# Optimization experiments

Hardware: AMD Instinct MI355X
Metric: run time of the kernel (lower is better)

Reference implementation:

```python
import jax, jax.numpy as jnp
import numpy as np

NUM_CLASSES = 2
THRESHOLD = 0.35
NEGPOS_RATIO = 7
VARIANCES = (0.1, 0.2)
B, P, O = 64, 16800, 64  # batch, num_priors, num_objs per image


def point_form(pr):
    # cxcywh -> xyxy
    return jnp.concatenate([pr[:, :2] - pr[:, 2:] / 2, pr[:, :2] + pr[:, 2:] / 2], axis=1)


def jaccard(a, b):
    # a: [A,4] xyxy, b: [Bx,4] xyxy -> IoU [A,Bx]
    lt = jnp.maximum(a[:, None, :2], b[None, :, :2])
    rb = jnp.minimum(a[:, None, 2:], b[None, :, 2:])
    wh = jnp.clip(rb - lt, 0.0)
    inter = wh[..., 0] * wh[..., 1]
    area_a = ((a[:, 2] - a[:, 0]) * (a[:, 3] - a[:, 1]))[:, None]
    area_b = ((b[:, 2] - b[:, 0]) * (b[:, 3] - b[:, 1]))[None, :]
    return inter / (area_a + area_b - inter)


def encode(matched, priors):
    # matched xyxy [P,4], priors cxcywh [P,4]
    g_cxcy = (matched[:, :2] + matched[:, 2:]) / 2 - priors[:, :2]
    g_cxcy = g_cxcy / (VARIANCES[0] * priors[:, 2:])
    g_wh = (matched[:, 2:] - matched[:, :2]) / priors[:, 2:]
    g_wh = jnp.log(g_wh) / VARIANCES[1]
    return jnp.concatenate([g_cxcy, g_wh], axis=1)


def encode_landm(matched, priors):
    # matched [P,10] -> [P,5,2]
    m = matched.reshape(-1, 5, 2)
    g = (m - priors[:, None, :2]) / (VARIANCES[0] * priors[:, None, 2:])
    return g.reshape(-1, 10)


def match_one(truths, labels, landms, priors):
    # truths [O,4], labels [O], landms [O,10]
    overlaps = jaccard(truths, point_form(priors))  # [O,P]
    best_prior_overlap = overlaps.max(axis=1)       # per-gt best IoU
    best_prior_idx = overlaps.argmax(axis=1)
    valid_gt = best_prior_overlap >= 0.2
    best_truth_overlap = overlaps.max(axis=0)       # per-prior best IoU
    best_truth_idx = overlaps.argmax(axis=0)
    # index_fill(2) only for valid gts (best_prior_idx_filter)
    bto = best_truth_overlap.at[best_prior_idx].set(
        jnp.where(valid_gt, 2.0, best_truth_overlap[best_prior_idx]))
    # ensure every gt keeps its best prior
    bti = best_truth_idx.at[best_prior_idx].set(jnp.arange(truths.shape[0]))
    matches = truths[bti]                  # [P,4]
    conf = labels[bti]                     # [P]
    conf = jnp.where(bto < THRESHOLD, 0.0, conf)
    loc = encode(matches, priors)
    landm = encode_landm(landms[bti], priors)
    return loc, conf, landm


def smooth_l1_sum(x, mask):
    ax = jnp.abs(x)
    v = jnp.where(ax < 1.0, 0.5 * ax * ax, ax - 0.5)
    return (v * mask).sum()


def setup_inputs() -> dict:
    key = jax.random.key(0)
    k1, k2, k3, k4, k5, k6, k7, k8 = jax.random.split(key, 8)
    loc_data = jax.random.normal(k1, (B, P, 4), jnp.float32)
    conf_data = jax.random.normal(k2, (B, P, NUM_CLASSES), jnp.float32)
    landm_data = jax.random.normal(k3, (B, P, 10), jnp.float32)
    # priors: cx,cy in (0,1), w,h in (0.02,0.22)
    cxy = jax.random.uniform(k4, (P, 2), jnp.float32)
    wh = jax.random.uniform(k5, (P, 2), jnp.float32) * 0.2 + 0.02
    priors = jnp.concatenate([cxy, wh], axis=1)
    # targets: valid corner boxes + landmarks + label in {1,-1}
    xy1 = jax.random.uniform(k6, (B, O, 2), jnp.float32) * 0.6
    bwh = jax.random.uniform(k7, (B, O, 2), jnp.float32) * 0.3 + 0.05
    boxes = jnp.concatenate([xy1, xy1 + bwh], axis=-1)
    lms = jax.random.uniform(k8, (B, O, 10), jnp.float32)
    lab = jnp.where(jax.random.uniform(jax.random.fold_in(key, 9), (B, O, 1)) < 0.3, -1.0, 1.0)
    targets = jnp.concatenate([boxes, lms, lab], axis=-1)
    return {"loc_data": loc_data, "conf_data": conf_data, "landm_data": landm_data,
            "priors": priors, "targets": targets}


def reference(loc_data, conf_data, landm_data, priors, targets):
    num = loc_data.shape[0]
    num_priors = priors.shape[0]
    truths = targets[:, :, :4]
    landms = targets[:, :, 4:14]
    labels = targets[:, :, -1]
    loc_t, conf_t, landm_t = jax.vmap(match_one, in_axes=(0, 0, 0, None))(
        truths, labels, landms, priors)  # [B,P,4], [B,P], [B,P,10]

    # landmark loss over conf_t > 0
    pos1 = conf_t > 0
    num_pos_landm = pos1.astype(jnp.int32).sum(axis=1, keepdims=True)
    N1 = jnp.maximum(num_pos_landm.sum().astype(jnp.float32), 1.0)
    loss_landm = smooth_l1_sum(landm_data - landm_t, pos1[..., None].astype(landm_data.dtype))

    # localization loss over conf_t != 0 ; conf_t[pos] = 1
    pos = conf_t != 0
    conf_t01 = jnp.where(pos, 1, 0)  # int {0,1}
    loss_l = smooth_l1_sum(loc_data - loc_t, pos[..., None].astype(loc_data.dtype))

    # hard negative mining on per-prior CE loss (global-max log_sum_exp, as in source)
    batch_conf = conf_data.reshape(-1, NUM_CLASSES)
    x_max = batch_conf.max()
    lse = jnp.log(jnp.exp(batch_conf - x_max).sum(axis=1, keepdims=True)) + x_max
    gathered = jnp.take_along_axis(batch_conf, conf_t01.reshape(-1, 1), axis=1)
    loss_c = (lse - gathered).reshape(num, -1)  # [B,P]; positives NOT zeroed (as in source)
    loss_idx = jnp.argsort(-loss_c, axis=1)
    idx_rank = jnp.argsort(loss_idx, axis=1)
    num_pos = pos.astype(jnp.int32).sum(axis=1, keepdims=True)  # [B,1]
    num_neg = jnp.minimum(NEGPOS_RATIO * num_pos, num_priors - 1)
    neg = idx_rank < num_neg  # [B,P]
    neg_pos = pos | neg

    # cross-entropy (sum) over selected pos+neg priors
    logp = jax.nn.log_softmax(conf_data, axis=-1)  # [B,P,C]
    ce = -jnp.take_along_axis(logp, conf_t01[..., None], axis=-1)[..., 0]
    loss_c_final = (ce * neg_pos.astype(ce.dtype)).sum()

    N = jnp.maximum(num_pos.sum().astype(jnp.float32), 1.0)
    return (loss_l / N, loss_c_final / N, loss_landm / N1)
```

## Files before the change

kernel.cpp:

```cpp
#include <hip/hip_runtime.h>
#include <math.h>

#define BN 64
#define PN 16800
#define ON 64
#define THRESH 0.35f
#define NEGPOS 7
#define GX 66
#define NBLK (BN * GX)
#define GXB 17
#define NBT (BN * GXB)
#define PT 4
#define TG 4
#define PSPLIT 2
#define PHALF 8400
#define NBP2 (BN * 16 * PSPLIT)
#define KREG 17
#define TAILV (PN - 16 * 1024)
#define NBINS 4096
#define MAXM 4096

struct GAcc {
  unsigned ticket;
  float sl, slm, sc;
  int np, np1;
  unsigned pad0, pad1;
};

__device__ __forceinline__ unsigned f2key(float f) {
  unsigned u = __float_as_uint(f);
  return (u & 0x80000000u) ? ~u : (u | 0x80000000u);
}
__device__ __forceinline__ float key2f(unsigned k) {
  unsigned u = (k & 0x80000000u) ? (k & 0x7FFFFFFFu) : ~k;
  return __uint_as_float(u);
}
__device__ __forceinline__ float sl1(float d) {
  float a = fabsf(d);
  return (a < 1.f) ? 0.5f * a * a : a - 0.5f;
}

__global__ void k_match2(const float* __restrict__ priors,
                         const float* __restrict__ targets,
                         float* __restrict__ bto, int* __restrict__ bti,
                         unsigned long long* __restrict__ bpp,
                         GAcc* __restrict__ gacc) {
  int bid = blockIdx.x;
  int tid = threadIdx.x;

  if (bid < NBT) {
    int b = bid / GXB;
    int slab = bid - b * GXB;
    int base = slab * 1024 + tid;
    if (bid == 0 && tid < 8)
      ((unsigned*)gacc)[tid] = 0;

    __shared__ float4 tbox[ON];
    __shared__ float tarea[ON];
    if (tid < ON) {
      const float* tg = &targets[((long)b * ON + tid) * 15];
      float4 bx = make_float4(tg[0], tg[1], tg[2], tg[3]);
      tbox[tid] = bx;
      tarea[tid] = (bx.z - bx.x) * (bx.w - bx.y);
    }
    __syncthreads();

    float px1[PT], py1[PT], px2[PT], py2[PT], ab[PT];
    bool val[PT];
#pragma unroll
    for (int i = 0; i < PT; i++) {
      int p = base + 256 * i;
      val[i] = p < PN;
      float4 pr = reinterpret_cast<const float4*>(priors)[val[i] ? p : base];
      px1[i] = pr.x - pr.z * 0.5f; py1[i] = pr.y - pr.w * 0.5f;
      px2[i] = pr.x + pr.z * 0.5f; py2[i] = pr.y + pr.w * 0.5f;
      ab[i] = (px2[i] - px1[i]) * (py2[i] - py1[i]);
    }
    float bi[PT], bu[PT]; int id[PT];
#pragma unroll
    for (int i = 0; i < PT; i++) { bi[i] = -1.f; bu[i] = 1.f; id[i] = 0; }

#pragma unroll 4
    for (int t = 0; t < ON; t++) {
      float4 a = tbox[t];
      float aa = tarea[t];
#pragma unroll
      for (int i = 0; i < PT; i++) {
        float lx = fmaxf(a.x, px1[i]), ly = fmaxf(a.y, py1[i]);
        float rx = fminf(a.z, px2[i]), ry = fminf(a.w, py2[i]);
        float w = fmaxf(rx - lx, 0.f), h = fmaxf(ry - ly, 0.f);
        float inter = w * h;
        float uni = aa + ab[i] - inter;
        if (inter * bu[i] > bi[i] * uni) { bi[i] = inter; bu[i] = uni; id[i] = t; }
      }
    }
#pragma unroll
    for (int i = 0; i < PT; i++) {
      if (val[i]) {
        int p = base + 256 * i;
        bto[(long)b * PN + p] = bi[i] / bu[i];
        bti[(long)b * PN + p] = id[i];
      }
    }
  } else {
    int id2 = bid - NBT;
    int b = id2 >> 5;
    int rest = id2 & 31;
    int g = rest >> 1;
    int h = rest & 1;
    int t0 = g * TG;
    float ax1[TG], ay1[TG], ax2[TG], ay2[TG], area_a[TG];
#pragma unroll
    for (int i = 0; i < TG; i++) {
      const float* tg = &targets[((long)b * ON + t0 + i) * 15];
      ax1[i] = tg[0]; ay1[i] = tg[1]; ax2[i] = tg[2]; ay2[i] = tg[3];
      area_a[i] = (ax2[i] - ax1[i]) * (ay2[i] - ay1[i]);
    }
    float bi[TG], bu[TG]; int bp[TG];
#pragma unroll
    for (int i = 0; i < TG; i++) { bi[i] = -1.f; bu[i] = 1.f; bp[i] = 0x7FFFFFFF; }
    int pend = (h + 1) * PHALF;
    for (int p = h * PHALF + tid; p < pend; p += 256) {
      float4 pr = reinterpret_cast<const float4*>(priors)[p];
      float px1 = pr.x - pr.z * 0.5f, py1 = pr.y - pr.w * 0.5f;
      float px2 = pr.x + pr.z * 0.5f, py2 = pr.y + pr.w * 0.5f;
      float area_b = (px2 - px1) * (py2 - py1);
#pragma unroll
      for (int i = 0; i < TG; i++) {
        float lx = fmaxf(ax1[i], px1), ly = fmaxf(ay1[i], py1);
        float rx = fminf(ax2[i], px2), ry = fminf(ay2[i], py2);
        float w = fmaxf(rx - lx, 0.f), h2 = fmaxf(ry - ly, 0.f);
        float inter = w * h2;
        float uni = area_a[i] + area_b - inter;
        if (inter * bu[i] > bi[i] * uni) { bi[i] = inter; bu[i] = uni; bp[i] = p; }
      }
    }
#pragma unroll
    for (int off = 1; off < 64; off <<= 1) {
#pragma unroll
      for (int i = 0; i < TG; i++) {
        float oi = __shfl_xor(bi[i], off), ou = __shfl_xor(bu[i], off);
        int op = __shfl_xor(bp[i], off);
        float a = oi * bu[i], c = bi[i] * ou;
        if (a > c || (a == c && op < bp[i])) { bi[i] = oi; bu[i] = ou; bp[i] = op; }
      }
    }
    __shared__ float si[TG][4], su[TG][4];
    __shared__ int spx[TG][4];
    int w = tid >> 6;
    if ((tid & 63) == 0) {
#pragma unroll
      for (int i = 0; i < TG; i++) { si[i][w] = bi[i]; su[i][w] = bu[i]; spx[i][w] = bp[i]; }
    }
    __syncthreads();
    if (tid < TG) {
      float fi = si[tid][0], fu = su[tid][0]; int fp = spx[tid][0];
      for (int ww = 1; ww < 4; ww++) {
        float a = si[tid][ww] * fu, c = fi * su[tid][ww];
        if (a > c || (a == c && spx[tid][ww] < fp)) { fi = si[tid][ww]; fu = su[tid][ww]; fp = spx[tid][ww]; }
      }
      float q = fi / fu;
      unsigned long long key = ((unsigned long long)f2key(q) << 32) | (unsigned)(~fp);
      bpp[((long)b * ON + t0 + tid) * PSPLIT + h] = key;
    }
  }
}

__global__ void k_encode(const float* __restrict__ loc_data,
                         const float* __restrict__ conf_data,
                         const float* __restrict__ landm_data,
                         const float* __restrict__ priors,
                         const float* __restrict__ targets,
                         const float* __restrict__ bto, const int* __restrict__ bti,
                         const unsigned long long* __restrict__ bpp,
                         float* __restrict__ lossc, unsigned char* __restrict__ posf,
                         float* __restrict__ part_l, float* __restrict__ part_lm,
                         int* __restrict__ np_part, int* __restrict__ np1_part) {
  int b = blockIdx.y;
  int p = blockIdx.x * 256 + threadIdx.x;
  int bid = b * GX + blockIdx.x;
  __shared__ float4 tgs4[ON * 15 / 4];
  __shared__ int ovr[256];
  float* tgs = (float*)tgs4;
  if (threadIdx.x < ON * 15 / 4)
    tgs4[threadIdx.x] = reinterpret_cast<const float4*>(targets + (long)b * ON * 15)[threadIdx.x];
  ovr[threadIdx.x] = -1;
  __syncthreads();
  if (threadIdx.x < ON) {
    int t = threadIdx.x;
    unsigned long long v0 = bpp[((long)b * ON + t) * PSPLIT];
    unsigned long long v1 = bpp[((long)b * ON + t) * PSPLIT + 1];
    unsigned long long best = v0 > v1 ? v0 : v1;
    float q = key2f((unsigned)(best >> 32));
    int qp = (int)(~(unsigned)best);
    int s0 = blockIdx.x * 256;
    if (qp >= s0 && qp < s0 + 256) {
      int valid = (q >= 0.2f) ? 1 : 0;
      atomicMax(&ovr[qp - s0], (t << 1) | valid);
    }
  }
  __syncthreads();

  float sum_l = 0.f, sum_lm = 0.f;
  int cp = 0, cp1 = 0;
  if (p < PN) {
    int t = bti[b * PN + p];
    float ov = bto[b * PN + p];
    int o = ovr[threadIdx.x];
    if (o >= 0) { t = o >> 1; if (o & 1) ov = 2.0f; }
    const float* tg = &tgs[t * 15];
    float label = tg[14];
    bool pos = ov >= THRESH;
    bool pos1 = pos && (label > 0.f);
    float4 pr = reinterpret_cast<const float4*>(priors)[p];
    if (pos) {
      float rz = 1.0f / pr.z, rw = 1.0f / pr.w;
      float m0 = tg[0], m1 = tg[1], m2 = tg[2], m3 = tg[3];
      float g0 = ((m0 + m2) * 0.5f - pr.x) * rz * 10.f;
      float g1 = ((m1 + m3) * 0.5f - pr.y) * rw * 10.f;
      float g2 = __logf((m2 - m0) * rz) * 5.f;
      float g3 = __logf((m3 - m1) * rw) * 5.f;
      const float* ld = &loc_data[((long)b * PN + p) * 4];
      sum_l = sl1(ld[0] - g0) + sl1(ld[1] - g1) + sl1(ld[2] - g2) + sl1(ld[3] - g3);
      cp = 1;
      if (pos1) {
        const float* lm = &landm_data[((long)b * PN + p) * 10];
#pragma unroll
        for (int i = 0; i < 5; i++) {
          float gx = (tg[4 + 2 * i] - pr.x) * rz * 10.f;
          float gy = (tg[5 + 2 * i] - pr.y) * rw * 10.f;
          sum_lm += sl1(lm[2 * i] - gx) + sl1(lm[2 * i + 1] - gy);
        }
        cp1 = 1;
      }
    }
    float2 c2 = reinterpret_cast<const float2*>(conf_data)[(long)b * PN + p];
    float m = fmaxf(c2.x, c2.y);
    float lse = m + __logf(__expf(c2.x - m) + __expf(c2.y - m));
    lossc[b * PN + p] = lse - (pos ? c2.y : c2.x);
    posf[b * PN + p] = pos ? 1 : 0;
  }
  for (int off = 32; off; off >>= 1) {
    sum_l += __shfl_down(sum_l, off);
    sum_lm += __shfl_down(sum_lm, off);
    cp += __shfl_down(cp, off);
    cp1 += __shfl_down(cp1, off);
  }
  __shared__ float sl4[4], slm4[4];
  __shared__ int sp4[4], sp14[4];
  int w = threadIdx.x >> 6;
  if ((threadIdx.x & 63) == 0) { sl4[w] = sum_l; slm4[w] = sum_lm; sp4[w] = cp; sp14[w] = cp1; }
  __syncthreads();
  if (threadIdx.x == 0) {
    part_l[bid] = sl4[0] + sl4[1] + sl4[2] + sl4[3];
    part_lm[bid] = slm4[0] + slm4[1] + slm4[2] + slm4[3];
    np_part[bid] = sp4[0] + sp4[1] + sp4[2] + sp4[3];
    np1_part[bid] = sp14[0] + sp14[1] + sp14[2] + sp14[3];
  }
}

__global__ void __launch_bounds__(1024) k_select(const float* __restrict__ lossc,
                                                 const unsigned char* __restrict__ posf,
                                                 const int* __restrict__ np_part,
                                                 const int* __restrict__ np1_part,
                                                 const float* __restrict__ part_l,
                                                 const float* __restrict__ part_lm,
                                                 GAcc* __restrict__ gacc,
                                                 float* __restrict__ out) {
  int b = blockIdx.x;
  int tid = threadIdx.x;
  int lane = tid & 63;
  int wv = tid >> 6;
  __shared__ unsigned hist[NBINS];
  __shared__ unsigned wtot[16];
  __shared__ float resv[MAXM];
  __shared__ int residx[MAXM];
  __shared__ int s_np, s_B, s_kp;
  __shared__ unsigned s_mc;
  const float* row = &lossc[(long)b * PN];
  const unsigned char* prow = &posf[(long)b * PN];

  if (tid == 0) s_np = 0;
  for (int i = tid; i < NBINS; i += 1024) hist[i] = 0;
  __syncthreads();
  if (tid < GX) atomicAdd(&s_np, np_part[b * GX + tid]);

  bool tailOk = tid < TAILV;
  float vreg[KREG];
  unsigned preg = 0;
#pragma unroll
  for (int r = 0; r < KREG - 1; r++) {
    vreg[r] = row[tid + 1024 * r];
    if (prow[tid + 1024 * r]) preg |= (1u << r);
  }
  vreg[KREG - 1] = tailOk ? row[tid + 1024 * (KREG - 1)] : -1.f;
  if (tailOk && prow[tid + 1024 * (KREG - 1)]) preg |= (1u << (KREG - 1));
  int breg[KREG];
#pragma unroll
  for (int r = 0; r < KREG; r++) {
    int q = (int)(vreg[r] * 256.0f);
    breg[r] = q < 0 ? 0 : (q > NBINS - 1 ? NBINS - 1 : q);
  }
  __syncthreads();
  int np = s_np;
  int k = NEGPOS * np;
  if (k > PN - 1) k = PN - 1;
  bool haveNeg = (k > 0);

  int B = NBINS, kp = 0, m = 0;
  bool allB = false, fallback = false;
  if (haveNeg) {
#pragma unroll
    for (int r = 0; r < KREG; r++)
      if (r < KREG - 1 || tailOk) atomicAdd(&hist[breg[r]], 1u);
    __syncthreads();
    int t4 = tid * 4;
    unsigned h0 = hist[t4], h1 = hist[t4 + 1], h2 = hist[t4 + 2], h3 = hist[t4 + 3];
    unsigned th = h0 + h1 + h2 + h3;
    unsigned v = th;
#pragma unroll
    for (int off = 1; off < 64; off <<= 1) {
      unsigned tv = (unsigned)__shfl_down((int)v, off);
      if (lane + off < 64) v += tv;
    }
    if (lane == 0) wtot[wv] = v;
    __syncthreads();
    unsigned add = 0;
    for (int w2 = wv + 1; w2 < 16; w2++) add += wtot[w2];
    unsigned S_t = v + add;
    unsigned S_next = S_t - th;
    if (S_t >= (unsigned)k && S_next < (unsigned)k) {
      unsigned run = S_next; int Bl; unsigned kpl;
      if (run + h3 >= (unsigned)k) { Bl = t4 + 3; kpl = k - run; }
      else { run += h3;
        if (run + h2 >= (unsigned)k) { Bl = t4 + 2; kpl = k - run; }
        else { run += h2;
          if (run + h1 >= (unsigned)k) { Bl = t4 + 1; kpl = k - run; }
          else { run += h1; Bl = t4; kpl = k - run; } } }
      s_B = Bl; s_kp = (int)kpl;
    }
    __syncthreads();
    B = s_B; kp = s_kp; m = (int)hist[B];
    allB = (kp == m);
    fallback = (!allB && m > MAXM);
  }

  float acc = 0.f;
  if (haveNeg && !allB && !fallback) {
    if (tid == 0) s_mc = 0;
    __syncthreads();
#pragma unroll
    for (int r = 0; r < KREG; r++) {
      if ((r < KREG - 1 || tailOk) && breg[r] == B) {
        unsigned slot = atomicAdd(&s_mc, 1u);
        resv[slot] = vreg[r];
        residx[slot] = (tid + 1024 * r) | (((preg >> r) & 1u) ? 0x40000000 : 0);
      }
    }
    __syncthreads();
    for (int i = tid; i < m; i += 1024) {
      float vi = resv[i];
      int pk = residx[i];
      int ii = pk & 0x3FFFFFFF;
      bool posi = (pk & 0x40000000) != 0;
      int rank = 0;
      for (int j = 0; j < m; j++) {
        float vj = resv[j];
        int ij = residx[j] & 0x3FFFFFFF;
        rank += (vj > vi || (vj == vi && ij < ii)) ? 1 : 0;
      }
      if (rank < kp && !posi) acc += vi;
    }
  }

  unsigned T = 0, R = 0, C = 0;
  if (fallback) {
    __shared__ unsigned s_lo, s_hi, fcnt[16];
    if (tid == 0) { s_lo = 0u; s_hi = 0xFFFFFFFFu; }
    __syncthreads();
    for (int it = 0; it < 32; it++) {
      unsigned lo = s_lo, hi = s_hi;
      unsigned mid = lo + ((hi - lo) >> 1) + ((hi - lo) & 1u);
      unsigned c = 0;
#pragma unroll
      for (int r = 0; r < KREG; r++)
        if (r < KREG - 1 || tailOk) c += (f2key(vreg[r]) >= mid) ? 1u : 0u;
#pragma unroll
      for (int o = 32; o; o >>= 1) c += (unsigned)__shfl_down((int)c, o);
      if (lane == 0) fcnt[wv] = c;
      __syncthreads();
      if (tid == 0) {
        unsigned tot = 0;
        for (int i = 0; i < 16; i++) tot += fcnt[i];
        if (tot >= (unsigned)k) s_lo = mid; else s_hi = mid - 1;
      }
      __syncthreads();
      if (s_lo >= s_hi) break;
    }
    T = s_lo;
    unsigned cg = 0, ce = 0;
#pragma unroll
    for (int r = 0; r < KREG; r++) {
      if (r < KREG - 1 || tailOk) {
        unsigned key = f2key(vreg[r]);
        cg += (key > T) ? 1u : 0u;
        ce += (key == T) ? 1u : 0u;
      }
    }
#pragma unroll
    for (int o = 32; o; o >>= 1) {
      cg += (unsigned)__shfl_down((int)cg, o);
      ce += (unsigned)__shfl_down((int)ce, o);
    }
    if (lane == 0) { fcnt[wv] = cg; wtot[wv] = ce; }
    __syncthreads();
    if (tid == 0) {
      unsigned tg2 = 0, te = 0;
      for (int i = 0; i < 16; i++) { tg2 += fcnt[i]; te += wtot[i]; }
      fcnt[0] = tg2; wtot[0] = te;
    }
    __syncthreads();
    C = wtot[0];
    R = (unsigned)k - fcnt[0];
    if (C != R && tid < 64) {
      unsigned running = 0;
      for (int base2 = 0; base2 < PN; base2 += 64) {
        int p = base2 + tid;
        bool tie = false, pos = false;
        float v2 = 0.f;
        if (p < PN) { v2 = row[p]; tie = (f2key(v2) == T); pos = prow[p] != 0; }
        unsigned long long mm = __ballot(tie);
        if (tie) {
          unsigned rank = running + (unsigned)__popcll(mm & ((1ull << tid) - 1));
          if (rank < R && !pos) acc += v2;
        }
        running += (unsigned)__popcll(mm);
      }
    }
  }

  unsigned ptc = 0;
#pragma unroll
  for (int r = 0; r < KREG; r++) {
    if (r < KREG - 1 || tailOk) {
      float v2 = vreg[r];
      bool pos = (preg >> r) & 1u;
      if (pos) acc += v2;
      else if (haveNeg) {
        if (!fallback) {
          if (breg[r] > B || (breg[r] == B && allB)) acc += v2;
        } else {
          if (f2key(v2) > T) acc += v2;
        }
      }
      if (fallback && pos && f2key(v2) == T) ptc++;
    }
  }
  for (int o = 32; o; o >>= 1) {
    acc += __shfl_down(acc, o);
    ptc += __shfl_down(ptc, o);
  }
  __shared__ float wsum[16];
  __shared__ unsigned wpt[16];
  if (lane == 0) { wsum[wv] = acc; wpt[wv] = ptc; }
  __syncthreads();

  __shared__ float s_rsl, s_rslm;
  __shared__ int s_rnp1;
  if (tid == 0) { s_rsl = 0.f; s_rslm = 0.f; s_rnp1 = 0; }
  __syncthreads();
  if (tid < GX) {
    atomicAdd(&s_rsl, part_l[b * GX + tid]);
    atomicAdd(&s_rslm, part_lm[b * GX + tid]);
    atomicAdd(&s_rnp1, np1_part[b * GX + tid]);
  }
  __syncthreads();

  if (tid == 0) {
    float tot = 0.f; unsigned pt = 0;
    for (int i = 0; i < 16; i++) { tot += wsum[i]; pt += wpt[i]; }
    if (fallback && C == R) tot += (float)(C - pt) * key2f(T);
    atomicAdd(&gacc->sc, tot);
    atomicAdd(&gacc->sl, s_rsl);
    atomicAdd(&gacc->slm, s_rslm);
    atomicAdd(&gacc->np, np);
    atomicAdd(&gacc->np1, s_rnp1);
  }
  __threadfence();
  __shared__ int lastF;
  if (tid == 0) lastF = (atomicAdd(&gacc->ticket, 1u) == (unsigned)(BN - 1)) ? 1 : 0;
  __syncthreads();
  if (lastF && tid == 0) {
    __threadfence();
    float sl = atomicAdd(&gacc->sl, 0.f);
    float slm = atomicAdd(&gacc->slm, 0.f);
    float sc = atomicAdd(&gacc->sc, 0.f);
    int tnp = atomicAdd(&gacc->np, 0);
    int tnp1 = atomicAdd(&gacc->np1, 0);
    float N = fmaxf((float)tnp, 1.f);
    float N1 = fmaxf((float)tnp1, 1.f);
    out[0] = sl / N;
    out[1] = sc / N;
    out[2] = slm / N1;
  }
}

extern "C" void kernel_launch(void* const* d_in, const int* in_sizes, int n_in,
                              void* d_out, int out_size, void* d_ws, size_t ws_size,
                              hipStream_t stream) {
  const float* loc_data = (const float*)d_in[0];
  const float* conf_data = (const float*)d_in[1];
  const float* landm_data = (const float*)d_in[2];
  const float* priors = (const float*)d_in[3];
  const float* targets = (const float*)d_in[4];
  float* out = (float*)d_out;

  char* ws = (char*)d_ws;
  const size_t SZ = (size_t)BN * PN * 4;
  size_t off = 0;
  float* lossc = (float*)(ws + off); off += SZ;
  float* bto = (float*)(ws + off); off += SZ;
  int* bti = (int*)(ws + off); off += SZ;
  unsigned char* posf = (unsigned char*)(ws + off); off += (size_t)BN * PN;
  off = (off + 15) & ~(size_t)15;
  unsigned long long* bpp = (unsigned long long*)(ws + off);
  off += (size_t)BN * ON * PSPLIT * 8;
  float* part_l = (float*)(ws + off); off += NBLK * 4;
  float* part_lm = (float*)(ws + off); off += NBLK * 4;
  int* np_part = (int*)(ws + off); off += NBLK * 4;
  int* np1_part = (int*)(ws + off); off += NBLK * 4;
  GAcc* gacc = (GAcc*)(ws + off); off += sizeof(GAcc);

  dim3 gbp(GX, BN);

  k_match2<<<NBT + NBP2, 256, 0, stream>>>(priors, targets, bto, bti, bpp, gacc);
  k_encode<<<gbp, 256, 0, stream>>>(loc_data, conf_data, landm_data, priors, targets,
                                    bto, bti, bpp, lossc, posf,
                                    part_l, part_lm, np_part, np1_part);
  k_select<<<BN, 1024, 0, stream>>>(lossc, posf, np_part, np1_part, part_l, part_lm,
                                    gacc, out);
}
```

Measured before the change: 209.4 us.

## Fuse encode stage into match kernel and apply best-prior overrides as deltas in select

Removes the separate k_encode kernel. The per-prior match blocks now compute the loc/landmark smooth-L1 partials, the per-prior CE loss and the positive flags directly from their own argmax results. The per-gt best-prior overrides are moved into k_select, which recomputes the changed priors' contributions as deltas and patches the loss and positive values through a shared-memory bitmap and lookup. This saves one launch and one global round trip over bto/bti, but adds serial fix-up work and a per-element bitmap check in the select kernel.

```diff
diff --git a/kernel.cpp b/kernel.cpp
--- a/kernel.cpp
+++ b/kernel.cpp
@@ -6,8 +6,6 @@
 #define ON 64
 #define THRESH 0.35f
 #define NEGPOS 7
-#define GX 66
-#define NBLK (BN * GX)
 #define GXB 17
 #define NBT (BN * GXB)
 #define PT 4
@@ -19,6 +17,7 @@
 #define TAILV (PN - 16 * 1024)
 #define NBINS 4096
 #define MAXM 4096
+#define BMW 525
 
 struct GAcc {
   unsigned ticket;
@@ -40,10 +39,44 @@
   return (a < 1.f) ? 0.5f * a * a : a - 0.5f;
 }
 
+__device__ __forceinline__ void contrib(const float* tg, float4 pr, float ov,
+                                        const float* ld, const float* lm,
+                                        float& l, float& lmv, int& cp, int& cp1) {
+  bool pos = ov >= THRESH;
+  float label = tg[14];
+  bool pos1 = pos && (label > 0.f);
+  l = 0.f; lmv = 0.f; cp = 0; cp1 = 0;
+  if (pos) {
+    float rz = 1.0f / pr.z, rw = 1.0f / pr.w;
+    float m0 = tg[0], m1 = tg[1], m2 = tg[2], m3 = tg[3];
+    float g0 = ((m0 + m2) * 0.5f - pr.x) * rz * 10.f;
+    float g1 = ((m1 + m3) * 0.5f - pr.y) * rw * 10.f;
+    float g2 = __logf((m2 - m0) * rz) * 5.f;
+    float g3 = __logf((m3 - m1) * rw) * 5.f;
+    l = sl1(ld[0] - g0) + sl1(ld[1] - g1) + sl1(ld[2] - g2) + sl1(ld[3] - g3);
+    cp = 1;
+    if (pos1) {
+#pragma unroll
+      for (int i = 0; i < 5; i++) {
+        float gx = (tg[4 + 2 * i] - pr.x) * rz * 10.f;
+        float gy = (tg[5 + 2 * i] - pr.y) * rw * 10.f;
+        lmv += sl1(lm[2 * i] - gx) + sl1(lm[2 * i + 1] - gy);
+      }
+      cp1 = 1;
+    }
+  }
+}
+
 __global__ void k_match2(const float* __restrict__ priors,
                          const float* __restrict__ targets,
+                         const float* __restrict__ loc_data,
+                         const float* __restrict__ conf_data,
+                         const float* __restrict__ landm_data,
                          float* __restrict__ bto, int* __restrict__ bti,
+                         float* __restrict__ lossc, unsigned char* __restrict__ posf,
                          unsigned long long* __restrict__ bpp,
+                         float* __restrict__ part_l, float* __restrict__ part_lm,
+                         int* __restrict__ np_part, int* __restrict__ np1_part,
                          GAcc* __restrict__ gacc) {
   int bid = blockIdx.x;
   int tid = threadIdx.x;
@@ -52,14 +85,18 @@
     int b = bid / GXB;
     int slab = bid - b * GXB;
     int base = slab * 1024 + tid;
-    if (bid == 0 && tid < 8)
-      ((unsigned*)gacc)[tid] = 0;
-
+    if (bid == 0 && tid < 8) ((unsigned*)gacc)[tid] = 0;
+
+    __shared__ float4 tgs4[ON * 15 / 4];
     __shared__ float4 tbox[ON];
     __shared__ float tarea[ON];
+    float* tgs = (float*)tgs4;
+    if (tid < ON * 15 / 4)
+      tgs4[tid] = reinterpret_cast<const float4*>(targets + (long)b * ON * 15)[tid];
+    __syncthreads();
     if (tid < ON) {
-      const float* tg = &targets[((long)b * ON + tid) * 15];
-      float4 bx = make_float4(tg[0], tg[1], tg[2], tg[3]);
+      float4 bx = make_float4(tgs[tid * 15], tgs[tid * 15 + 1],
+                              tgs[tid * 15 + 2], tgs[tid * 15 + 3]);
       tbox[tid] = bx;
       tarea[tid] = (bx.z - bx.x) * (bx.w - bx.y);
     }
@@ -94,13 +131,47 @@
         if (inter * bu[i] > bi[i] * uni) { bi[i] = inter; bu[i] = uni; id[i] = t; }
       }
     }
+
+    float sum_l = 0.f, sum_lm = 0.f;
+    int cp = 0, cp1 = 0;
 #pragma unroll
     for (int i = 0; i < PT; i++) {
       if (val[i]) {
         int p = base + 256 * i;
-        bto[(long)b * PN + p] = bi[i] / bu[i];
-        bti[(long)b * PN + p] = id[i];
-      }
+        long gp = (long)b * PN + p;
+        float ov = bi[i] / bu[i];
+        int t = id[i];
+        bto[gp] = ov;
+        bti[gp] = t;
+        float4 pr = reinterpret_cast<const float4*>(priors)[p];
+        float l, lmv; int c0, c1;
+        contrib(&tgs[t * 15], pr, ov, &loc_data[gp * 4], &landm_data[gp * 10],
+                l, lmv, c0, c1);
+        sum_l += l; sum_lm += lmv; cp += c0; cp1 += c1;
+        float2 c2 = reinterpret_cast<const float2*>(conf_data)[gp];
+        float m = fmaxf(c2.x, c2.y);
+        float lse = m + __logf(__expf(c2.x - m) + __expf(c2.y - m));
+        bool pos = ov >= THRESH;
+        lossc[gp] = lse - (pos ? c2.y : c2.x);
+        posf[gp] = pos ? 1 : 0;
+      }
+    }
+    for (int off = 32; off; off >>= 1) {
+      sum_l += __shfl_down(sum_l, off);
+      sum_lm += __shfl_down(sum_lm, off);
+      cp += __shfl_down(cp, off);
+      cp1 += __shfl_down(cp1, off);
+    }
+    __shared__ float sl4[4], slm4[4];
+    __shared__ int sp4[4], sp14[4];
+    int w = tid >> 6;
+    if ((tid & 63) == 0) { sl4[w] = sum_l; slm4[w] = sum_lm; sp4[w] = cp; sp14[w] = cp1; }
+    __syncthreads();
+    if (tid == 0) {
+      part_l[bid] = sl4[0] + sl4[1] + sl4[2] + sl4[3];
+      part_lm[bid] = slm4[0] + slm4[1] + slm4[2] + slm4[3];
+      np_part[bid] = sp4[0] + sp4[1] + sp4[2] + sp4[3];
+      np1_part[bid] = sp14[0] + sp14[1] + sp14[2] + sp14[3];
     }
   } else {
     int id2 = bid - NBT;
@@ -166,101 +237,16 @@
   }
 }
 
-__global__ void k_encode(const float* __restrict__ loc_data,
-                         const float* __restrict__ conf_data,
-                         const float* __restrict__ landm_data,
-                         const float* __restrict__ priors,
-                         const float* __restrict__ targets,
-                         const float* __restrict__ bto, const int* __restrict__ bti,
-                         const unsigned long long* __restrict__ bpp,
-                         float* __restrict__ lossc, unsigned char* __restrict__ posf,
-                         float* __restrict__ part_l, float* __restrict__ part_lm,
-                         int* __restrict__ np_part, int* __restrict__ np1_part) {
-  int b = blockIdx.y;
-  int p = blockIdx.x * 256 + threadIdx.x;
-  int bid = b * GX + blockIdx.x;
-  __shared__ float4 tgs4[ON * 15 / 4];
-  __shared__ int ovr[256];
-  float* tgs = (float*)tgs4;
-  if (threadIdx.x < ON * 15 / 4)
-    tgs4[threadIdx.x] = reinterpret_cast<const float4*>(targets + (long)b * ON * 15)[threadIdx.x];
-  ovr[threadIdx.x] = -1;
-  __syncthreads();
-  if (threadIdx.x < ON) {
-    int t = threadIdx.x;
-    unsigned long long v0 = bpp[((long)b * ON + t) * PSPLIT];
-    unsigned long long v1 = bpp[((long)b * ON + t) * PSPLIT + 1];
-    unsigned long long best = v0 > v1 ? v0 : v1;
-    float q = key2f((unsigned)(best >> 32));
-    int qp = (int)(~(unsigned)best);
-    int s0 = blockIdx.x * 256;
-    if (qp >= s0 && qp < s0 + 256) {
-      int valid = (q >= 0.2f) ? 1 : 0;
-      atomicMax(&ovr[qp - s0], (t << 1) | valid);
-    }
-  }
-  __syncthreads();
-
-  float sum_l = 0.f, sum_lm = 0.f;
-  int cp = 0, cp1 = 0;
-  if (p < PN) {
-    int t = bti[b * PN + p];
-    float ov = bto[b * PN + p];
-    int o = ovr[threadIdx.x];
-    if (o >= 0) { t = o >> 1; if (o & 1) ov = 2.0f; }
-    const float* tg = &tgs[t * 15];
-    float label = tg[14];
-    bool pos = ov >= THRESH;
-    bool pos1 = pos && (label > 0.f);
-    float4 pr = reinterpret_cast<const float4*>(priors)[p];
-    if (pos) {
-      float rz = 1.0f / pr.z, rw = 1.0f / pr.w;
-      float m0 = tg[0], m1 = tg[1], m2 = tg[2], m3 = tg[3];
-      float g0 = ((m0 + m2) * 0.5f - pr.x) * rz * 10.f;
-      float g1 = ((m1 + m3) * 0.5f - pr.y) * rw * 10.f;
-      float g2 = __logf((m2 - m0) * rz) * 5.f;
-      float g3 = __logf((m3 - m1) * rw) * 5.f;
-      const float* ld = &loc_data[((long)b * PN + p) * 4];
-      sum_l = sl1(ld[0] - g0) + sl1(ld[1] - g1) + sl1(ld[2] - g2) + sl1(ld[3] - g3);
-      cp = 1;
-      if (pos1) {
-        const float* lm = &landm_data[((long)b * PN + p) * 10];
-#pragma unroll
-        for (int i = 0; i < 5; i++) {
-          float gx = (tg[4 + 2 * i] - pr.x) * rz * 10.f;
-          float gy = (tg[5 + 2 * i] - pr.y) * rw * 10.f;
-          sum_lm += sl1(lm[2 * i] - gx) + sl1(lm[2 * i + 1] - gy);
-        }
-        cp1 = 1;
-      }
-    }
-    float2 c2 = reinterpret_cast<const float2*>(conf_data)[(long)b * PN + p];
-    float m = fmaxf(c2.x, c2.y);
-    float lse = m + __logf(__expf(c2.x - m) + __expf(c2.y - m));
-    lossc[b * PN + p] = lse - (pos ? c2.y : c2.x);
-    posf[b * PN + p] = pos ? 1 : 0;
-  }
-  for (int off = 32; off; off >>= 1) {
-    sum_l += __shfl_down(sum_l, off);
-    sum_lm += __shfl_down(sum_lm, off);
-    cp += __shfl_down(cp, off);
-    cp1 += __shfl_down(cp1, off);
-  }
-  __shared__ float sl4[4], slm4[4];
-  __shared__ int sp4[4], sp14[4];
-  int w = threadIdx.x >> 6;
-  if ((threadIdx.x & 63) == 0) { sl4[w] = sum_l; slm4[w] = sum_lm; sp4[w] = cp; sp14[w] = cp1; }
-  __syncthreads();
-  if (threadIdx.x == 0) {
-    part_l[bid] = sl4[0] + sl4[1] + sl4[2] + sl4[3];
-    part_lm[bid] = slm4[0] + slm4[1] + slm4[2] + slm4[3];
-    np_part[bid] = sp4[0] + sp4[1] + sp4[2] + sp4[3];
-    np1_part[bid] = sp14[0] + sp14[1] + sp14[2] + sp14[3];
-  }
-}
-
 __global__ void __launch_bounds__(1024) k_select(const float* __restrict__ lossc,
                                                  const unsigned char* __restrict__ posf,
+                                                 const float* __restrict__ priors,
+                                                 const float* __restrict__ targets,
+                                                 const float* __restrict__ loc_data,
+                                                 const float* __restrict__ conf_data,
+                                                 const float* __restrict__ landm_data,
+                                                 const float* __restrict__ bto,
+                                                 const int* __restrict__ bti,
+                                                 const unsigned long long* __restrict__ bpp,
                                                  const int* __restrict__ np_part,
                                                  const int* __restrict__ np1_part,
                                                  const float* __restrict__ part_l,
@@ -275,6 +261,12 @@
   __shared__ unsigned wtot[16];
   __shared__ float resv[MAXM];
   __shared__ int residx[MAXM];
+  __shared__ unsigned bitmap[BMW];
+  __shared__ int fixq[ON];
+  __shared__ float fixv[ON];
+  __shared__ unsigned char fixp[ON];
+  __shared__ float s_dl, s_dlm;
+  __shared__ int s_dnp, s_dnp1;
   __shared__ int s_np, s_B, s_kp;
   __shared__ unsigned s_mc;
   const float* row = &lossc[(long)b * PN];
@@ -282,27 +274,82 @@
 
   if (tid == 0) s_np = 0;
   for (int i = tid; i < NBINS; i += 1024) hist[i] = 0;
+  for (int i = tid; i < BMW; i += 1024) bitmap[i] = 0;
   __syncthreads();
-  if (tid < GX) atomicAdd(&s_np, np_part[b * GX + tid]);
+
+  if (tid < ON) {
+    int t = tid;
+    unsigned long long v0 = bpp[((long)b * ON + t) * PSPLIT];
+    unsigned long long v1 = bpp[((long)b * ON + t) * PSPLIT + 1];
+    unsigned long long best = v0 > v1 ? v0 : v1;
+    float q = key2f((unsigned)(best >> 32));
+    int qp = (int)(~(unsigned)best);
+    bool valid = q >= 0.2f;
+    bool dupLater = false;
+    for (int j = 0; j < 64; j++) {
+      int ij = __shfl(qp, j);
+      if (j > t && ij == qp) dupLater = true;
+    }
+    float dl = 0.f, dlm = 0.f; int dnp = 0, dnp1 = 0;
+    fixq[t] = -1;
+    if (!dupLater) {
+      long gp = (long)b * PN + qp;
+      float ov_old = bto[gp];
+      int t_old = bti[gp];
+      float ov_new = valid ? 2.0f : ov_old;
+      int t_new = t;
+      float4 pr = reinterpret_cast<const float4*>(priors)[qp];
+      const float* ld = &loc_data[gp * 4];
+      const float* lm = &landm_data[gp * 10];
+      float lo, lmo, ln2, lmn; int co, c1o, cn, c1n;
+      contrib(&targets[((long)b * ON + t_old) * 15], pr, ov_old, ld, lm, lo, lmo, co, c1o);
+      contrib(&targets[((long)b * ON + t_new) * 15], pr, ov_new, ld, lm, ln2, lmn, cn, c1n);
+      dl = ln2 - lo; dlm = lmn - lmo; dnp = cn - co; dnp1 = c1n - c1o;
+      float2 c2 = reinterpret_cast<const float2*>(conf_data)[gp];
+      float m = fmaxf(c2.x, c2.y);
+      float lse = m + __logf(__expf(c2.x - m) + __expf(c2.y - m));
+      bool pos_new = ov_new >= THRESH;
+      fixq[t] = qp;
+      fixv[t] = lse - (pos_new ? c2.y : c2.x);
+      fixp[t] = pos_new ? 1 : 0;
+      atomicOr(&bitmap[qp >> 5], 1u << (qp & 31));
+    }
+    for (int off = 32; off; off >>= 1) {
+      dl += __shfl_down(dl, off);
+      dlm += __shfl_down(dlm, off);
+      dnp += __shfl_down(dnp, off);
+      dnp1 += __shfl_down(dnp1, off);
+    }
+    if (t == 0) { s_dl = dl; s_dlm = dlm; s_dnp = dnp; s_dnp1 = dnp1; }
+  } else if (tid >= 64 && tid < 64 + GXB) {
+    atomicAdd(&s_np, np_part[b * GXB + (tid - 64)]);
+  }
+  __syncthreads();
 
   bool tailOk = tid < TAILV;
   float vreg[KREG];
   unsigned preg = 0;
 #pragma unroll
-  for (int r = 0; r < KREG - 1; r++) {
-    vreg[r] = row[tid + 1024 * r];
-    if (prow[tid + 1024 * r]) preg |= (1u << r);
-  }
-  vreg[KREG - 1] = tailOk ? row[tid + 1024 * (KREG - 1)] : -1.f;
-  if (tailOk && prow[tid + 1024 * (KREG - 1)]) preg |= (1u << (KREG - 1));
+  for (int r = 0; r < KREG; r++) {
+    int p = tid + 1024 * r;
+    bool ok = (r < KREG - 1) || tailOk;
+    float v = ok ? row[p] : -1.f;
+    bool ps = ok ? (prow[p] != 0) : false;
+    if (ok && (bitmap[p >> 5] & (1u << (p & 31)))) {
+      for (int j = 0; j < ON; j++) {
+        if (fixq[j] == p) { v = fixv[j]; ps = fixp[j] != 0; }
+      }
+    }
+    vreg[r] = v;
+    if (ps) preg |= (1u << r);
+  }
   int breg[KREG];
 #pragma unroll
   for (int r = 0; r < KREG; r++) {
     int q = (int)(vreg[r] * 256.0f);
     breg[r] = q < 0 ? 0 : (q > NBINS - 1 ? NBINS - 1 : q);
   }
-  __syncthreads();
-  int np = s_np;
+  int np = s_np + s_dnp;
   int k = NEGPOS * np;
   if (k > PN - 1) k = PN - 1;
   bool haveNeg = (k > 0);
@@ -428,7 +475,15 @@
         int p = base2 + tid;
         bool tie = false, pos = false;
         float v2 = 0.f;
-        if (p < PN) { v2 = row[p]; tie = (f2key(v2) == T); pos = prow[p] != 0; }
+        if (p < PN) {
+          v2 = row[p];
+          pos = prow[p] != 0;
+          if (bitmap[p >> 5] & (1u << (p & 31))) {
+            for (int j = 0; j < ON; j++)
+              if (fixq[j] == p) { v2 = fixv[j]; pos = fixp[j] != 0; }
+          }
+          tie = (f2key(v2) == T);
+        }
         unsigned long long mm = __ballot(tie);
         if (tie) {
           unsigned rank = running + (unsigned)__popcll(mm & ((1ull << tid) - 1));
@@ -467,12 +522,12 @@
 
   __shared__ float s_rsl, s_rslm;
   __shared__ int s_rnp1;
-  if (tid == 0) { s_rsl = 0.f; s_rslm = 0.f; s_rnp1 = 0; }
+  if (tid == 0) { s_rsl = s_dl; s_rslm = s_dlm; s_rnp1 = s_dnp1; }
   __syncthreads();
-  if (tid < GX) {
-    atomicAdd(&s_rsl, part_l[b * GX + tid]);
-    atomicAdd(&s_rslm, part_lm[b * GX + tid]);
-    atomicAdd(&s_rnp1, np1_part[b * GX + tid]);
+  if (tid < GXB) {
+    atomicAdd(&s_rsl, part_l[b * GXB + tid]);
+    atomicAdd(&s_rslm, part_lm[b * GXB + tid]);
+    atomicAdd(&s_rnp1, np1_part[b * GXB + tid]);
   }
   __syncthreads();
 
@@ -525,18 +580,16 @@
   off = (off + 15) & ~(size_t)15;
   unsigned long long* bpp = (unsigned long long*)(ws + off);
   off += (size_t)BN * ON * PSPLIT * 8;
-  float* part_l = (float*)(ws + off); off += NBLK * 4;
-  float* part_lm = (float*)(ws + off); off += NBLK * 4;
-  int* np_part = (int*)(ws + off); off += NBLK * 4;
-  int* np1_part = (int*)(ws + off); off += NBLK * 4;
+  float* part_l = (float*)(ws + off); off += NBT * 4;
+  float* part_lm = (float*)(ws + off); off += NBT * 4;
+  int* np_part = (int*)(ws + off); off += NBT * 4;
+  int* np1_part = (int*)(ws + off); off += NBT * 4;
   GAcc* gacc = (GAcc*)(ws + off); off += sizeof(GAcc);
 
-  dim3 gbp(GX, BN);
-
-  k_match2<<<NBT + NBP2, 256, 0, stream>>>(priors, targets, bto, bti, bpp, gacc);
-  k_encode<<<gbp, 256, 0, stream>>>(loc_data, conf_data, landm_data, priors, targets,
-                                    bto, bti, bpp, lossc, posf,
-                                    part_l, part_lm, np_part, np1_part);
-  k_select<<<BN, 1024, 0, stream>>>(lossc, posf, np_part, np1_part, part_l, part_lm,
-                                    gacc, out);
-}
+  k_match2<<<NBT + NBP2, 256, 0, stream>>>(priors, targets, loc_data, conf_data,
+                                           landm_data, bto, bti, lossc, posf, bpp,
+                                           part_l, part_lm, np_part, np1_part, gacc);
+  k_select<<<BN, 1024, 0, stream>>>(lossc, posf, priors, targets, loc_data,
+                                    conf_data, landm_data, bto, bti, bpp,
+                                    np_part, np1_part, part_l, part_lm, gacc, out);
+}
```

New measurement: 223.3 us. +6.6%, slower.
